# Optimization experiments

Measured on AMD Instinct MI355X. Metric: run time of the kernel, lower is better.

Reference implementation:

```python
import jax, jax.numpy as jnp
import numpy as np

DIM = 512
BATCH = 64
SRC_L = 2048


def setup_inputs() -> dict:
    key = jax.random.key(0)
    ks = jax.random.split(key, 7)
    s = 1.0 / np.sqrt(DIM)
    return {
        "query": jax.random.normal(ks[0], (BATCH, DIM), dtype=jnp.float32),
        "ref": jax.random.normal(ks[1], (SRC_L, BATCH, DIM), dtype=jnp.float32),
        # nn.Linear(dim, dim)
        "Wq": jax.random.uniform(ks[2], (DIM, DIM), jnp.float32, -s, s),
        "bq": jax.random.uniform(ks[3], (DIM,), jnp.float32, -s, s),
        # nn.Conv1d(dim, dim, 1, 1) -> weight [out, in, 1] squeezed to [out, in]
        "Wr": jax.random.uniform(ks[4], (DIM, DIM), jnp.float32, -s, s),
        "br": jax.random.uniform(ks[5], (DIM,), jnp.float32, -s, s),
        # self.v ~ U(-1/sqrt(dim), 1/sqrt(dim))
        "v": jax.random.uniform(ks[6], (DIM,), jnpp := jnp.float32, -s, s),
    }


def reference(query, ref, Wq, bq, Wr, br, v):
    # ref: [L, B, D] -> [B, D, L]
    ref_bdl = jnp.transpose(ref, (1, 2, 0))
    # q = Linear(query): [B, D] -> broadcast as [B, D, 1]
    q = query @ Wq.T + bq  # [B, D]
    # e = 1x1 Conv1d over ref: pointwise GEMM along channel dim
    e = jnp.einsum("oi,bil->bol", Wr, ref_bdl) + br[None, :, None]  # [B, D, L]
    # u = v . tanh(q + e) reduced over D (fused broadcast-add-tanh-reduce)
    u = jnp.einsum("d,bdl->bl", v, jnp.tanh(q[:, :, None] + e))  # [B, L]
    logits = u  # use_tanh=False
    return (e, logits)
```

## Files before the change

kernel.cpp:

```cpp
#include <hip/hip_runtime.h>

#define DIM 512
#define B_  64
#define L_  2048

typedef unsigned short u16;
typedef float f32x4 __attribute__((ext_vector_type(4)));
typedef short s16x8 __attribute__((ext_vector_type(8)));
typedef short s16x4 __attribute__((ext_vector_type(4)));

__device__ __forceinline__ u16 f2bf(float f) {
  union { float f; unsigned u; } x{f};
  unsigned r = x.u + 0x7FFFu + ((x.u >> 16) & 1u);
  return (u16)(r >> 16);
}

__device__ __forceinline__ float tanh_fast(float x) {
  float e2 = __expf(2.0f * x);
  return 1.0f - 2.0f / (e2 + 1.0f);
}

__global__ __launch_bounds__(256) void prep_kernel(
    const float* __restrict__ query, const float* __restrict__ Wq,
    const float* __restrict__ bq, const float* __restrict__ Wr,
    float* __restrict__ q_out, u16* __restrict__ Wrbt) {
  const int blk = blockIdx.x;
  const int tid = threadIdx.x;
  if (blk < 64) {
    __shared__ float qs[DIM];
    for (int i = tid; i < DIM; i += 256) qs[i] = query[blk * DIM + i];
    __syncthreads();
    for (int o = tid; o < DIM; o += 256) {
      const float* w = Wq + o * DIM;
      float acc = 0.f;
      for (int k = 0; k < DIM; k += 4) {
        f32x4 a = *(const f32x4*)&qs[k];
        f32x4 b = *(const f32x4*)&w[k];
        acc += a.x * b.x + a.y * b.y + a.z * b.z + a.w * b.w;
      }
      q_out[blk * DIM + o] = acc + bq[o];
    }
  } else {
    const int c = blk - 64;
    const int flat = c * 4096 + tid * 16;
    const int o = flat >> 9, k0 = flat & 511;
    const int t = k0 >> 5, kk = k0 & 31;
    u16* dst = Wrbt + t * 16384 + o * 32 + kk;
#pragma unroll
    for (int i = 0; i < 4; ++i) {
      f32x4 a = *(const f32x4*)&Wr[flat + i * 4];
      s16x4 o4;
      o4.x = (short)f2bf(a.x); o4.y = (short)f2bf(a.y);
      o4.z = (short)f2bf(a.z); o4.w = (short)f2bf(a.w);
      *(s16x4*)&dst[i * 4] = o4;
    }
  }
}

__global__ __launch_bounds__(512, 3) void gemm_fused(
    const float* __restrict__ ref, const u16* __restrict__ Wrbt,
    const float* __restrict__ q, const float* __restrict__ br,
    const float* __restrict__ v, float* __restrict__ e_out,
    float* __restrict__ logits) {
  __shared__ u16 Bs[32 * 520];
  __shared__ float u_lds[8][32];

  const int b = blockIdx.x, lc = blockIdx.y;
  const int l0 = lc * 32;
  const int tid = threadIdx.x, lane = tid & 63, w = tid >> 6;
  const int rr = lane & 15, kg = lane >> 4;

#pragma unroll
  for (int p = 0; p < 8; ++p) {
    const int row = p * 4 + (tid >> 7);
    const int col4 = tid & 127;
    f32x4 a = __builtin_nontemporal_load(
        (const f32x4*)&ref[((size_t)(l0 + row) * 64 + b) * 512 + col4 * 4]);
    s16x4 o4;
    o4.x = (short)f2bf(a.x); o4.y = (short)f2bf(a.y);
    o4.z = (short)f2bf(a.z); o4.w = (short)f2bf(a.w);
    const int unit = row * 65 + ((col4 >> 1) ^ ((row & 7) << 2));
    *(s16x4*)&Bs[(unit << 3) + ((col4 & 1) << 2)] = o4;
  }
  __syncthreads();

  const u16* ap = Wrbt + (w * 64 + rr) * 32 + kg * 8;

  f32x4 acc[4][2];
#pragma unroll
  for (int fm = 0; fm < 4; ++fm)
#pragma unroll
    for (int fn = 0; fn < 2; ++fn) acc[fm][fn] = (f32x4){0.f, 0.f, 0.f, 0.f};

  s16x8 A0[4], A1[4];
#pragma unroll
  for (int fm = 0; fm < 4; ++fm) {
    A0[fm] = *(const s16x8*)(ap + 0 * 16384 + fm * 512);
    A1[fm] = *(const s16x8*)(ap + 1 * 16384 + fm * 512);
  }

#pragma unroll
  for (int t = 0; t < 16; ++t) {
    s16x8 bf[2];
#pragma unroll
    for (int fn = 0; fn < 2; ++fn) {
      const int row = fn * 16 + rr;
      const int unit = row * 65 + ((t * 4 + kg) ^ ((row & 7) << 2));
      bf[fn] = *(const s16x8*)&Bs[unit << 3];
    }
    if (t & 1) {
#pragma unroll
      for (int fm = 0; fm < 4; ++fm)
#pragma unroll
        for (int fn = 0; fn < 2; ++fn)
          acc[fm][fn] = __builtin_amdgcn_mfma_f32_16x16x32_bf16(bf[fn], A1[fm], acc[fm][fn], 0, 0, 0);
      if (t + 2 < 16)
#pragma unroll
        for (int fm = 0; fm < 4; ++fm)
          A1[fm] = *(const s16x8*)(ap + (t + 2) * 16384 + fm * 512);
    } else {
#pragma unroll
      for (int fm = 0; fm < 4; ++fm)
#pragma unroll
        for (int fn = 0; fn < 2; ++fn)
          acc[fm][fn] = __builtin_amdgcn_mfma_f32_16x16x32_bf16(bf[fn], A0[fm], acc[fm][fn], 0, 0, 0);
      if (t + 2 < 16)
#pragma unroll
        for (int fm = 0; fm < 4; ++fm)
          A0[fm] = *(const s16x8*)(ap + (t + 2) * 16384 + fm * 512);
    }
  }

  f32x4 usA[2];
#pragma unroll
  for (int fn = 0; fn < 2; ++fn) usA[fn] = (f32x4){0.f, 0.f, 0.f, 0.f};
#pragma unroll
  for (int fm = 0; fm < 4; ++fm) {
    const int o = w * 64 + fm * 16 + rr;
    const float brv = br[o];
    const float qv = q[b * DIM + o] + brv;
    const float vv = v[o];
    const size_t erow = ((size_t)(b * DIM + o)) * L_;
#pragma unroll
    for (int fn = 0; fn < 2; ++fn) {
      const int lb = l0 + fn * 16 + kg * 4;
      f32x4 a = acc[fm][fn];
      f32x4 ev = a + brv;
      *(f32x4*)&e_out[erow + lb] = ev;
      f32x4 th;
      th.x = tanh_fast(a.x + qv);
      th.y = tanh_fast(a.y + qv);
      th.z = tanh_fast(a.z + qv);
      th.w = tanh_fast(a.w + qv);
      usA[fn] += vv * th;
    }
  }
#pragma unroll
  for (int fn = 0; fn < 2; ++fn) {
    f32x4 us = usA[fn];
#pragma unroll
    for (int msk = 1; msk <= 8; msk <<= 1) {
      us.x += __shfl_xor(us.x, msk);
      us.y += __shfl_xor(us.y, msk);
      us.z += __shfl_xor(us.z, msk);
      us.w += __shfl_xor(us.w, msk);
    }
    if (rr == 0)
      *(f32x4*)&u_lds[w][fn * 16 + kg * 4] = us;
  }
  __syncthreads();
  if (tid < 32) {
    float s = 0.f;
#pragma unroll
    for (int ww = 0; ww < 8; ++ww) s += u_lds[ww][tid];
    logits[(size_t)b * L_ + l0 + tid] = s;
  }
}

extern "C" void kernel_launch(void* const* d_in, const int* in_sizes, int n_in,
                              void* d_out, int out_size, void* d_ws, size_t ws_size,
                              hipStream_t stream) {
  const float* query = (const float*)d_in[0];
  const float* ref   = (const float*)d_in[1];
  const float* Wq    = (const float*)d_in[2];
  const float* bq    = (const float*)d_in[3];
  const float* Wr    = (const float*)d_in[4];
  const float* br    = (const float*)d_in[5];
  const float* v     = (const float*)d_in[6];

  float* e_out  = (float*)d_out;
  float* logits = e_out + (size_t)B_ * DIM * L_;

  char* ws = (char*)d_ws;
  u16*   Wrbt = (u16*)ws;
  float* q    = (float*)(ws + 524288);

  prep_kernel<<<128, 256, 0, stream>>>(query, Wq, bq, Wr, q, Wrbt);
  gemm_fused<<<dim3(64, 64), 512, 0, stream>>>(ref, Wrbt, q, br, v, e_out, logits);
}
```

Measured before the change: 242.3 us.

## Retile GEMM over output-channel groups with double-buffered ref staging and LDS-staged e stores

Each block now covers a 128-output-channel group and 128 sequence positions, where before it covered all 512 channels and 32 positions. The ref tile is streamed in 32-wide K chunks through a double-buffered LDS slab, with the next chunk's global loads overlapping the current MFMAs. The e output is transposed through LDS so the nontemporal stores are long contiguous rows along L instead of short 16-byte fragments. Partial logits per channel group go to a workspace and a new small kernel reduces them. Each ref element is now loaded four times (once per channel group), there is a sync per K step, and an extra kernel launch is added.

```diff
diff --git a/kernel.cpp b/kernel.cpp
--- a/kernel.cpp
+++ b/kernel.cpp
@@ -57,34 +57,41 @@
   }
 }
 
-__global__ __launch_bounds__(512, 3) void gemm_fused(
+__global__ __launch_bounds__(512, 4) void gemm_fused(
     const float* __restrict__ ref, const u16* __restrict__ Wrbt,
     const float* __restrict__ q, const float* __restrict__ br,
     const float* __restrict__ v, float* __restrict__ e_out,
-    float* __restrict__ logits) {
-  __shared__ u16 Bs[32 * 520];
-  __shared__ float u_lds[8][32];
-
-  const int b = blockIdx.x, lc = blockIdx.y;
-  const int l0 = lc * 32;
+    float* __restrict__ upart) {
+  __shared__ u16 Bs[2][128 * 40];
+  __shared__ float u_lds[2][128];
+
+  const int bidx = blockIdx.x;
+  const int og = bidx & 3, b = (bidx >> 2) & 63, lt = bidx >> 8;
+
   const int tid = threadIdx.x, lane = tid & 63, w = tid >> 6;
+  const int wo = w >> 2, wl = w & 3;
   const int rr = lane & 15, kg = lane >> 4;
 
-#pragma unroll
-  for (int p = 0; p < 8; ++p) {
-    const int row = p * 4 + (tid >> 7);
-    const int col4 = tid & 127;
-    f32x4 a = __builtin_nontemporal_load(
-        (const f32x4*)&ref[((size_t)(l0 + row) * 64 + b) * 512 + col4 * 4]);
-    s16x4 o4;
-    o4.x = (short)f2bf(a.x); o4.y = (short)f2bf(a.y);
-    o4.z = (short)f2bf(a.z); o4.w = (short)f2bf(a.w);
-    const int unit = row * 65 + ((col4 >> 1) ^ ((row & 7) << 2));
-    *(s16x4*)&Bs[(unit << 3) + ((col4 & 1) << 2)] = o4;
+  {
+    f32x4 sr[2];
+#pragma unroll
+    for (int p = 0; p < 2; ++p) {
+      const int g = p * 512 + tid, row = g >> 3, c8 = g & 7;
+      sr[p] = __builtin_nontemporal_load(
+          (const f32x4*)&ref[((size_t)(lt * 128 + row) * 64 + b) * 512 + c8 * 4]);
+    }
+#pragma unroll
+    for (int p = 0; p < 2; ++p) {
+      const int g = p * 512 + tid, row = g >> 3, c8 = g & 7;
+      s16x4 o4;
+      o4.x = (short)f2bf(sr[p].x); o4.y = (short)f2bf(sr[p].y);
+      o4.z = (short)f2bf(sr[p].z); o4.w = (short)f2bf(sr[p].w);
+      *(s16x4*)&Bs[0][row * 40 + c8 * 4] = o4;
+    }
   }
   __syncthreads();
 
-  const u16* ap = Wrbt + (w * 64 + rr) * 32 + kg * 8;
+  const u16* ap = Wrbt + (og * 128 + wo * 64 + rr) * 32 + kg * 8;
 
   f32x4 acc[4][2];
 #pragma unroll
@@ -92,61 +99,57 @@
 #pragma unroll
     for (int fn = 0; fn < 2; ++fn) acc[fm][fn] = (f32x4){0.f, 0.f, 0.f, 0.f};
 
-  s16x8 A0[4], A1[4];
+  for (int t = 0; t < 16; ++t) {
+    f32x4 sr[2];
+    if (t < 15) {
+#pragma unroll
+      for (int p = 0; p < 2; ++p) {
+        const int g = p * 512 + tid, row = g >> 3, c8 = g & 7;
+        sr[p] = __builtin_nontemporal_load(
+            (const f32x4*)&ref[((size_t)(lt * 128 + row) * 64 + b) * 512 + (t + 1) * 32 + c8 * 4]);
+      }
+    }
+    s16x8 af[4];
+#pragma unroll
+    for (int fm = 0; fm < 4; ++fm)
+      af[fm] = *(const s16x8*)(ap + t * 16384 + fm * 512);
+    s16x8 bf[2];
+#pragma unroll
+    for (int fn = 0; fn < 2; ++fn) {
+      const int row = wl * 32 + fn * 16 + rr;
+      bf[fn] = *(const s16x8*)&Bs[t & 1][row * 40 + kg * 8];
+    }
+#pragma unroll
+    for (int fm = 0; fm < 4; ++fm)
+#pragma unroll
+      for (int fn = 0; fn < 2; ++fn)
+        acc[fm][fn] = __builtin_amdgcn_mfma_f32_16x16x32_bf16(bf[fn], af[fm], acc[fm][fn], 0, 0, 0);
+    if (t < 15) {
+#pragma unroll
+      for (int p = 0; p < 2; ++p) {
+        const int g = p * 512 + tid, row = g >> 3, c8 = g & 7;
+        s16x4 o4;
+        o4.x = (short)f2bf(sr[p].x); o4.y = (short)f2bf(sr[p].y);
+        o4.z = (short)f2bf(sr[p].z); o4.w = (short)f2bf(sr[p].w);
+        *(s16x4*)&Bs[(t + 1) & 1][row * 40 + c8 * 4] = o4;
+      }
+    }
+    __syncthreads();
+  }
+
+  float bb[4];
+  f32x4 usA[2];
+#pragma unroll
+  for (int fn = 0; fn < 2; ++fn) usA[fn] = (f32x4){0.f, 0.f, 0.f, 0.f};
 #pragma unroll
   for (int fm = 0; fm < 4; ++fm) {
-    A0[fm] = *(const s16x8*)(ap + 0 * 16384 + fm * 512);
-    A1[fm] = *(const s16x8*)(ap + 1 * 16384 + fm * 512);
-  }
-
-#pragma unroll
-  for (int t = 0; t < 16; ++t) {
-    s16x8 bf[2];
+    const int o = og * 128 + wo * 64 + fm * 16 + rr;
+    bb[fm] = br[o];
+    const float qv = q[b * DIM + o] + bb[fm];
+    const float vv = v[o];
 #pragma unroll
     for (int fn = 0; fn < 2; ++fn) {
-      const int row = fn * 16 + rr;
-      const int unit = row * 65 + ((t * 4 + kg) ^ ((row & 7) << 2));
-      bf[fn] = *(const s16x8*)&Bs[unit << 3];
-    }
-    if (t & 1) {
-#pragma unroll
-      for (int fm = 0; fm < 4; ++fm)
-#pragma unroll
-        for (int fn = 0; fn < 2; ++fn)
-          acc[fm][fn] = __builtin_amdgcn_mfma_f32_16x16x32_bf16(bf[fn], A1[fm], acc[fm][fn], 0, 0, 0);
-      if (t + 2 < 16)
-#pragma unroll
-        for (int fm = 0; fm < 4; ++fm)
-          A1[fm] = *(const s16x8*)(ap + (t + 2) * 16384 + fm * 512);
-    } else {
-#pragma unroll
-      for (int fm = 0; fm < 4; ++fm)
-#pragma unroll
-        for (int fn = 0; fn < 2; ++fn)
-          acc[fm][fn] = __builtin_amdgcn_mfma_f32_16x16x32_bf16(bf[fn], A0[fm], acc[fm][fn], 0, 0, 0);
-      if (t + 2 < 16)
-#pragma unroll
-        for (int fm = 0; fm < 4; ++fm)
-          A0[fm] = *(const s16x8*)(ap + (t + 2) * 16384 + fm * 512);
-    }
-  }
-
-  f32x4 usA[2];
-#pragma unroll
-  for (int fn = 0; fn < 2; ++fn) usA[fn] = (f32x4){0.f, 0.f, 0.f, 0.f};
-#pragma unroll
-  for (int fm = 0; fm < 4; ++fm) {
-    const int o = w * 64 + fm * 16 + rr;
-    const float brv = br[o];
-    const float qv = q[b * DIM + o] + brv;
-    const float vv = v[o];
-    const size_t erow = ((size_t)(b * DIM + o)) * L_;
-#pragma unroll
-    for (int fn = 0; fn < 2; ++fn) {
-      const int lb = l0 + fn * 16 + kg * 4;
       f32x4 a = acc[fm][fn];
-      f32x4 ev = a + brv;
-      *(f32x4*)&e_out[erow + lb] = ev;
       f32x4 th;
       th.x = tanh_fast(a.x + qv);
       th.y = tanh_fast(a.y + qv);
@@ -166,15 +169,46 @@
       us.w += __shfl_xor(us.w, msk);
     }
     if (rr == 0)
-      *(f32x4*)&u_lds[w][fn * 16 + kg * 4] = us;
-  }
-  __syncthreads();
-  if (tid < 32) {
-    float s = 0.f;
-#pragma unroll
-    for (int ww = 0; ww < 8; ++ww) s += u_lds[ww][tid];
-    logits[(size_t)b * L_ + l0 + tid] = s;
-  }
+      *(f32x4*)&u_lds[wo][wl * 32 + fn * 16 + kg * 4] = us;
+  }
+
+  float* Ebuf = (float*)&Bs[0][0];
+#pragma unroll
+  for (int ph = 0; ph < 4; ++ph) {
+    if (wo == (ph >> 1)) {
+      const int fmb = (ph & 1) * 2;
+#pragma unroll
+      for (int f2 = 0; f2 < 2; ++f2) {
+        const int fm = fmb + f2;
+        const int op = f2 * 16 + rr;
+#pragma unroll
+        for (int fn = 0; fn < 2; ++fn) {
+          const int l = wl * 32 + fn * 16 + kg * 4;
+          f32x4 ev = acc[fm][fn] + bb[fm];
+          *(f32x4*)&Ebuf[op * 132 + l] = ev;
+        }
+      }
+    }
+    __syncthreads();
+#pragma unroll
+    for (int i = 0; i < 2; ++i) {
+      const int flat = (w * 2 + i) * 256 + lane * 4;
+      const int op = flat >> 7, lcol = flat & 127;
+      f32x4 ev = *(const f32x4*)&Ebuf[op * 132 + lcol];
+      __builtin_nontemporal_store(
+          ev, (f32x4*)&e_out[((size_t)(b * DIM + og * 128 + ph * 32 + op)) * L_ + lt * 128 + lcol]);
+    }
+    __syncthreads();
+  }
+
+  if (tid < 128)
+    upart[(size_t)(og * 64 + b) * L_ + lt * 128 + tid] = u_lds[0][tid] + u_lds[1][tid];
+}
+
+__global__ __launch_bounds__(256) void ured_kernel(
+    const float* __restrict__ up, float* __restrict__ out) {
+  const int idx = blockIdx.x * 256 + threadIdx.x;
+  out[idx] = up[idx] + up[idx + 131072] + up[idx + 262144] + up[idx + 393216];
 }
 
 extern "C" void kernel_launch(void* const* d_in, const int* in_sizes, int n_in,
@@ -192,9 +226,11 @@
   float* logits = e_out + (size_t)B_ * DIM * L_;
 
   char* ws = (char*)d_ws;
-  u16*   Wrbt = (u16*)ws;
-  float* q    = (float*)(ws + 524288);
+  u16*   Wrbt  = (u16*)ws;
+  float* q     = (float*)(ws + 524288);
+  float* upart = (float*)(ws + 655360);
 
   prep_kernel<<<128, 256, 0, stream>>>(query, Wq, bq, Wr, q, Wrbt);
-  gemm_fused<<<dim3(64, 64), 512, 0, stream>>>(ref, Wrbt, q, br, v, e_out, logits);
-}
+  gemm_fused<<<4096, 512, 0, stream>>>(ref, Wrbt, q, br, v, e_out, upart);
+  ured_kernel<<<512, 256, 0, stream>>>(upart, logits);
+}
```

Measured after the change: 317.9 us. 31.2% more time.
